# Kernel tuning notes

Measured on AMD Instinct MI355X. Metric: run time of the kernel, lower is better.

The kernel has to match this reference:

```python
import jax, jax.numpy as jnp
import numpy as np
from jax import lax

DIM = 96
B, S = 2, 48
EPS_LN = 1e-6
EPS_GRN = 1e-6


def setup_inputs() -> dict:
    key = jax.random.key(0)
    ks = jax.random.split(key, 11)
    d, h = DIM, 4 * DIM
    return {
        "x": jax.random.normal(ks[0], (B, d, S, S, S), jnp.float32),
        "dw_w": jax.random.normal(ks[1], (d, 1, 7, 7, 7), jnp.float32) * 0.05,  # (O, I/groups, kD,kH,kW)
        "dw_b": jax.random.normal(ks[2], (d,), jnp.float32) * 0.02,
        "ln_w": jnp.ones((d,), jnp.float32),
        "ln_b": jnp.zeros((d,), jnp.float32),
        "w1": jax.random.normal(ks[3], (d, h), jnp.float32) * 0.02,
        "b1": jax.random.normal(ks[4], (h,), jnp.float32) * 0.02,
        "grn_w": jax.random.normal(ks[5], (h,), jnp.float32) * 0.02,
        "grn_b": jax.random.normal(ks[6], (h,), jnp.float32) * 0.02,
        "w2": jax.random.normal(ks[7], (h, d), jnp.float32) * 0.02,
        "b2": jax.random.normal(ks[8], (d,), jnp.float32) * 0.02,
    }


def reference(x, dw_w, dw_b, ln_w, ln_b, w1, b1, grn_w, grn_b, w2, b2):
    # depthwise 7x7x7 conv, padding 3, groups = channels; x: (B, C, D, H, W)
    y = lax.conv_general_dilated(
        x, dw_w, window_strides=(1, 1, 1), padding=[(3, 3)] * 3,
        dimension_numbers=("NCDHW", "OIDHW", "NCDHW"), feature_group_count=DIM,
    ) + dw_b[None, :, None, None, None]
    # channels_last: (B, D, H, W, C)
    h = jnp.transpose(y, (0, 2, 3, 4, 1))
    # LayerNorm over channel dim
    mu = jnp.mean(h, axis=-1, keepdims=True)
    var = jnp.mean((h - mu) ** 2, axis=-1, keepdims=True)
    h = (h - mu) * lax.rsqrt(var + EPS_LN) * ln_w + ln_b
    # pointwise MLP expand + GELU (exact, erf-based, like torch)
    h = jnp.einsum("bdhwc,ce->bdhwe", h, w1) + b1
    h = jax.nn.gelu(h, approximate=False)
    # GRN: global L2 norm over spatial dims (1,2,3), per channel
    g = jnp.sqrt(jnp.sum(h * h, axis=(1, 2, 3), keepdims=True))  # (B,1,1,1,4C)
    n = g / (jnp.mean(g, axis=-1, keepdims=True) + EPS_GRN)
    h = grn_w * (h * n) + grn_b + h
    # pointwise MLP contract
    h = jnp.einsum("bdhwe,ec->bdhwc", h, w2) + b2
    # back to channels_first + residual
    return x + jnp.transpose(h, (0, 4, 1, 2, 3))
```

## Files before the change

kernel.cpp:

```cpp
#include <hip/hip_runtime.h>
#include <hip/hip_bf16.h>
#include <string.h>

#define S3 110592
#define CDIM 96
#define EDIM 384
#define ZIN 14
#define YIN 22

typedef __attribute__((ext_vector_type(8))) short bf16x8;
typedef __attribute__((ext_vector_type(4))) float f32x4;
typedef unsigned short ushort_t;

__device__ __forceinline__ ushort_t f2bf(float f) {
  __hip_bfloat16 h = __float2bfloat16(f);
  union { __hip_bfloat16 h; ushort_t u; } cv; cv.h = h; return cv.u;
}
__device__ __forceinline__ float bf2f(ushort_t u) {
  union { __hip_bfloat16 h; ushort_t u; } cv; cv.u = u; return __bfloat162float(cv.h);
}

__global__ void kprep(const float* __restrict__ ln_w, const float* __restrict__ ln_b,
                      const float* __restrict__ w1, const float* __restrict__ b1,
                      const float* __restrict__ grn_b, const float* __restrict__ w2,
                      const float* __restrict__ b2,
                      ushort_t* __restrict__ w1p, float* __restrict__ b1f, float* __restrict__ bias2) {
  int idx = blockIdx.x * 256 + threadIdx.x;
  if (idx < 24 * 3 * 64 * 8) {
    int j = idx & 7, lane = (idx >> 3) & 63, ks = (idx >> 9) % 3, nt = idx / 1536;
    int c = ks * 32 + (lane >> 4) * 8 + j;
    int e = nt * 16 + (lane & 15);
    w1p[idx] = f2bf(ln_w[c] * w1[c * EDIM + e]);
  }
  if (idx < EDIM) {
    float s = b1[idx];
    for (int c = 0; c < CDIM; ++c) s += ln_b[c] * w1[c * EDIM + idx];
    b1f[idx] = s;
  }
  if (idx < CDIM) {
    float s = b2[idx];
    for (int e = 0; e < EDIM; ++e) s += grn_b[e] * w2[e * CDIM + idx];
    bias2[idx] = s;
  }
}

__global__ void kpackB(const float* __restrict__ dw_w, ushort_t* __restrict__ Btab) {
  int idx = blockIdx.x * 256 + threadIdx.x;
  if (idx >= 96 * 49 * 512) return;
  int pos = idx & 511; int t = (idx >> 9) % 49; int c = idx / (49 * 512);
  int lane = pos >> 3, j = pos & 7;
  int k = (lane >> 4) * 8 + j, n = lane & 15;
  int tx = k - n - 1;
  int tz = t / 7, ty = t % 7;
  float v = (tx >= 0 && tx < 7) ? dw_w[c * 343 + tz * 49 + ty * 7 + tx] : 0.f;
  Btab[idx] = f2bf(v);
}

template<int HALF>
__device__ __forceinline__ void conv_ty_loop(const unsigned* tile, const ushort_t* Bt,
                                             int lane, int am, int xg, f32x4* acc) {
#pragma unroll 1
  for (int ty = 0; ty < 7; ++ty) {
    bf16x8 bfr[7];
#pragma unroll
    for (int tz = 0; tz < 7; ++tz)
      bfr[tz] = *(const bf16x8*)&Bt[(tz * 7 + ty) * 512 + lane * 8];
    int rowbase = am + ty;
#pragma unroll
    for (int zl = 0; zl < 7; ++zl) {
      int row = (HALF * 7 + zl) * YIN + rowbase;
      int byteoff = (row << 7) + (xg ^ ((row & 7) << 4));
      bf16x8 af = *(const bf16x8*)((const char*)tile + byteoff);
#pragma unroll
      for (int tz = 0; tz < 7; ++tz) {
        int l = (HALF == 0) ? (zl - tz) : (zl + 6 - tz);
        if (l >= 0 && l < 7)
          acc[l] = __builtin_amdgcn_mfma_f32_16x16x32_bf16(af, bfr[tz], acc[l], 0, 0, 0);
      }
    }
  }
}

__global__ __launch_bounds__(384, 6) void kconv(const float* __restrict__ x,
                                                const ushort_t* __restrict__ Btab,
                                                const float* __restrict__ dw_b,
                                                ushort_t* __restrict__ y) {
  __shared__ unsigned tile[ZIN * YIN * 32];
  int bid = blockIdx.x;
  int xcd = bid & 7, wi = bid >> 3;
  int c = xcd * 12 + wi / 36;
  int rr_ = wi % 36;
  int b = rr_ / 18;
  int t_ = rr_ % 18;
  int zt = t_ / 3, yt = t_ % 3;
  int z0 = zt * 8, y0 = yt * 16;
  size_t base = (size_t)(b * 96 + c) * S3;
  int tid = threadIdx.x;

  for (int i = tid; i < 308 * 8; i += 384) {
    int row = i >> 3; int pe = i & 7;
    int pc = (pe < 2) ? pe : pe + 24;
    tile[(row << 5) + (pc ^ ((row & 7) << 2))] = 0u;
  }
#pragma unroll 4
  for (int i = tid; i < 308 * 24; i += 384) {
    int row = i / 24; int pc = 2 + (i - row * 24);
    int dz = row / YIN, dy = row - dz * YIN;
    int gz = z0 - 3 + dz, gy = y0 - 3 + dy;
    float2 v = make_float2(0.f, 0.f);
    if ((unsigned)gz < 48u && (unsigned)gy < 48u)
      v = *(const float2*)&x[base + (size_t)gz * 2304 + gy * 48 + 2 * pc - 4];
    tile[(row << 5) + (pc ^ ((row & 7) << 2))] = (unsigned)f2bf(v.x) | ((unsigned)f2bf(v.y) << 16);
  }
  __syncthreads();

  int w = tid >> 6;
  int X = w % 3, half = w / 3;
  int lane = tid & 63;
  int am = lane & 15, g = lane >> 4;
  int xg = X * 32 + g * 16;

  f32x4 acc[7];
#pragma unroll
  for (int p = 0; p < 7; ++p) acc[p] = (f32x4){0.f, 0.f, 0.f, 0.f};

  const ushort_t* __restrict__ Bt = Btab + (size_t)c * 49 * 512;
  if (half == 0) conv_ty_loop<0>(tile, Bt, lane, am, xg, acc);
  else           conv_ty_loop<1>(tile, Bt, lane, am, xg, acc);

  float bv = dw_b[c];
  float* red = (float*)tile;
  int rcol = X * 16 + am;
  __syncthreads();
  if (half == 0) {
#pragma unroll
    for (int l = 1; l < 7; ++l)
#pragma unroll
      for (int r = 0; r < 4; ++r)
        red[(l - 1) * 800 + (g * 4 + r) * 50 + rcol] = acc[l][r];
  }
  __syncthreads();
  if (half == 0) {
    size_t zb = base + (size_t)z0 * 2304;
#pragma unroll
    for (int r = 0; r < 4; ++r)
      y[zb + (size_t)(y0 + g * 4 + r) * 48 + rcol] = f2bf(acc[0][r] + bv);
  } else {
#pragma unroll
    for (int l = 0; l < 7; ++l) {
      size_t zb = base + (size_t)(z0 + l + 1) * 2304;
#pragma unroll
      for (int r = 0; r < 4; ++r) {
        float v = acc[l][r] + bv;
        if (l < 6) v += red[l * 800 + (g * 4 + r) * 50 + rcol];
        y[zb + (size_t)(y0 + g * 4 + r) * 48 + rcol] = f2bf(v);
      }
    }
  }
}

__global__ __launch_bounds__(512, 4) void kmlp1(const ushort_t* __restrict__ y,
                                                const ushort_t* __restrict__ w1p,
                                                const float* __restrict__ b1f,
                                                ushort_t* __restrict__ h,
                                                float* __restrict__ sumsq) {
  __shared__ ushort_t Al[64 * 104];
  __shared__ float red_s[8][64], red_q[8][64];
  __shared__ float stat_mu[64], stat_rv[64];
  __shared__ float ssq_s[EDIM];
  int tid = threadIdx.x;
  int q = tid >> 6, lane = tid & 63;
  size_t pos0 = (size_t)blockIdx.x * 64;
  int b = (int)(pos0 / S3);
  int sp0 = (int)(pos0 % S3);

  bf16x8 bfg[3][3];
#pragma unroll
  for (int ntl = 0; ntl < 3; ++ntl)
#pragma unroll
    for (int ks = 0; ks < 3; ++ks)
      bfg[ntl][ks] = *(const bf16x8*)&w1p[(size_t)(((q * 3 + ntl) * 3 + ks) * 64 + lane) * 8];

  float v[12];
  float s = 0.f, ss = 0.f;
  const ushort_t* yb = y + (size_t)b * 96 * S3 + sp0 + lane;
#pragma unroll
  for (int i = 0; i < 12; ++i) {
    float f = bf2f(yb[(size_t)(q * 12 + i) * S3]);
    v[i] = f; s += f; ss += f * f;
  }
  red_s[q][lane] = s; red_q[q][lane] = ss;
  __syncthreads();
  if (tid < 64) {
    float su = 0.f, sq = 0.f;
#pragma unroll
    for (int k = 0; k < 8; ++k) { su += red_s[k][tid]; sq += red_q[k][tid]; }
    float mu = su * (1.f / 96.f);
    float var = sq * (1.f / 96.f) - mu * mu;
    stat_mu[tid] = mu;
    stat_rv[tid] = rsqrtf(var + 1e-6f);
  }
  __syncthreads();
  {
    float mu = stat_mu[lane], rv = stat_rv[lane];
#pragma unroll
    for (int i4 = 0; i4 < 3; ++i4) {
      ushort_t u0 = f2bf((v[i4 * 4 + 0] - mu) * rv);
      ushort_t u1 = f2bf((v[i4 * 4 + 1] - mu) * rv);
      ushort_t u2 = f2bf((v[i4 * 4 + 2] - mu) * rv);
      ushort_t u3 = f2bf((v[i4 * 4 + 3] - mu) * rv);
      uint2 t; t.x = (unsigned)u0 | ((unsigned)u1 << 16); t.y = (unsigned)u2 | ((unsigned)u3 << 16);
      *(uint2*)&Al[lane * 104 + q * 12 + i4 * 4] = t;
    }
  }
  __syncthreads();

  f32x4 acc[4][3];
#pragma unroll
  for (int mt = 0; mt < 4; ++mt)
#pragma unroll
    for (int ntl = 0; ntl < 3; ++ntl) acc[mt][ntl] = (f32x4){0.f, 0.f, 0.f, 0.f};

  int row = lane & 15, g = lane >> 4;
#pragma unroll
  for (int ks = 0; ks < 3; ++ks) {
    bf16x8 af[4];
    int colb = ks * 32 + g * 8;
#pragma unroll
    for (int mt = 0; mt < 4; ++mt)
      af[mt] = *(const bf16x8*)&Al[(mt * 16 + row) * 104 + colb];
#pragma unroll
    for (int ntl = 0; ntl < 3; ++ntl) {
#pragma unroll
      for (int mt = 0; mt < 4; ++mt)
        acc[mt][ntl] = __builtin_amdgcn_mfma_f32_16x16x32_bf16(af[mt], bfg[ntl][ks], acc[mt][ntl], 0, 0, 0);
    }
  }

#pragma unroll
  for (int ntl = 0; ntl < 3; ++ntl) {
    int e = q * 48 + ntl * 16 + row;
    float bb = b1f[e];
    float ssq = 0.f;
#pragma unroll
    for (int mt = 0; mt < 4; ++mt) {
#pragma unroll
      for (int r = 0; r < 4; ++r) {
        float val = acc[mt][ntl][r] + bb;
        float gel = 0.5f * val * (1.f + erff(val * 0.70710678118f));
        size_t p = pos0 + mt * 16 + g * 4 + r;
        h[p * EDIM + e] = f2bf(gel);
        ssq += gel * gel;
      }
    }
    ssq += __shfl_xor(ssq, 16, 64);
    ssq += __shfl_xor(ssq, 32, 64);
    if (g == 0) ssq_s[e] = ssq;
  }
  __syncthreads();
  if (tid < EDIM) atomicAdd(&sumsq[b * EDIM + tid], ssq_s[tid]);
}

__global__ void kscale(const float* __restrict__ sumsq, const float* __restrict__ grn_w,
                       float* __restrict__ scale) {
  __shared__ float wsum[6];
  __shared__ float mean_s;
  int b = blockIdx.x, e = threadIdx.x;
  float gv = sqrtf(sumsq[b * EDIM + e]);
  float t = gv;
#pragma unroll
  for (int off = 1; off <= 32; off <<= 1) t += __shfl_xor(t, off, 64);
  if ((e & 63) == 0) wsum[e >> 6] = t;
  __syncthreads();
  if (e == 0) {
    float m = 0.f;
    for (int i = 0; i < 6; ++i) m += wsum[i];
    mean_s = m * (1.f / EDIM);
  }
  __syncthreads();
  scale[b * EDIM + e] = grn_w[e] * (gv / (mean_s + 1e-6f)) + 1.f;
}

__global__ void kpackw2(const float* __restrict__ scale, const float* __restrict__ w2,
                        ushort_t* __restrict__ w2s) {
  int idx = blockIdx.x * 256 + threadIdx.x;
  int b = idx / 36864; int r = idx % 36864;
  int j = r & 7, lane = (r >> 3) & 63, ks = (r >> 9) % 12, nt = r / 6144;
  int e = ks * 32 + (lane >> 4) * 8 + j, cc = nt * 16 + (lane & 15);
  w2s[idx] = f2bf(scale[b * EDIM + e] * w2[e * CDIM + cc]);
}

__global__ __launch_bounds__(256, 4) void kmlp2(const ushort_t* __restrict__ h,
                                                const ushort_t* __restrict__ w2s,
                                                const float* __restrict__ bias2,
                                                const float* __restrict__ x,
                                                float* __restrict__ out) {
  __shared__ float tile[96 * 65];
  int tid = threadIdx.x;
  int w = tid >> 6, lane = tid & 63;
  size_t pos0 = (size_t)blockIdx.x * 128;
  int b = (int)(pos0 / S3);
  int sp0 = (int)(pos0 % S3);
  int row = lane & 15, g = lane >> 4;

  f32x4 acc[2][6];
#pragma unroll
  for (int hf = 0; hf < 2; ++hf)
#pragma unroll
    for (int nt = 0; nt < 6; ++nt) acc[hf][nt] = (f32x4){0.f, 0.f, 0.f, 0.f};

  const ushort_t* w2b = w2s + (size_t)b * 36864;
  size_t abase0 = (pos0 + w * 16 + row) * (size_t)EDIM + g * 8;
  size_t abase1 = abase0 + (size_t)64 * EDIM;
#pragma unroll
  for (int ks = 0; ks < 12; ++ks) {
    bf16x8 af0 = *(const bf16x8*)&h[abase0 + ks * 32];
    bf16x8 af1 = *(const bf16x8*)&h[abase1 + ks * 32];
#pragma unroll
    for (int nt = 0; nt < 6; ++nt) {
      bf16x8 bfg = *(const bf16x8*)&w2b[(size_t)((nt * 12 + ks) * 64 + lane) * 8];
      acc[0][nt] = __builtin_amdgcn_mfma_f32_16x16x32_bf16(af0, bfg, acc[0][nt], 0, 0, 0);
      acc[1][nt] = __builtin_amdgcn_mfma_f32_16x16x32_bf16(af1, bfg, acc[1][nt], 0, 0, 0);
    }
  }

#pragma unroll
  for (int hf = 0; hf < 2; ++hf) {
    __syncthreads();
#pragma unroll
    for (int nt = 0; nt < 6; ++nt) {
      int cc = nt * 16 + row;
#pragma unroll
      for (int r = 0; r < 4; ++r)
        tile[cc * 65 + w * 16 + g * 4 + r] = acc[hf][nt][r];
    }
    __syncthreads();
#pragma unroll
    for (int k = 0; k < 12; ++k) {
      int idx = tid + k * 256;
      int cc = idx >> 5, pp = (idx & 31) * 2;
      size_t o = (size_t)(b * 96 + cc) * S3 + sp0 + hf * 64 + pp;
      float2 xv = *(const float2*)&x[o];
      float bb = bias2[cc];
      float2 ov;
      ov.x = xv.x + tile[cc * 65 + pp] + bb;
      ov.y = xv.y + tile[cc * 65 + pp + 1] + bb;
      *(float2*)&out[o] = ov;
    }
  }
}

extern "C" void kernel_launch(void* const* d_in, const int* in_sizes, int n_in,
                              void* d_out, int out_size, void* d_ws, size_t ws_size,
                              hipStream_t stream) {
  const float* x     = (const float*)d_in[0];
  const float* dw_w  = (const float*)d_in[1];
  const float* dw_b  = (const float*)d_in[2];
  const float* ln_w  = (const float*)d_in[3];
  const float* ln_b  = (const float*)d_in[4];
  const float* w1    = (const float*)d_in[5];
  const float* b1    = (const float*)d_in[6];
  const float* grn_w = (const float*)d_in[7];
  const float* grn_b = (const float*)d_in[8];
  const float* w2    = (const float*)d_in[9];
  const float* b2    = (const float*)d_in[10];
  float* out = (float*)d_out;

  char* ws = (char*)d_ws;
  size_t off = 0;
  auto alloc = [&](size_t bytes) -> void* {
    void* p = ws + off;
    off = (off + bytes + 511) & ~(size_t)511;
    return p;
  };
  ushort_t* y    = (ushort_t*)alloc((size_t)2 * 96 * S3 * 2);
  ushort_t* h    = (ushort_t*)alloc((size_t)221184 * EDIM * 2);
  ushort_t* w1p  = (ushort_t*)alloc(36864 * 2);
  ushort_t* w2s  = (ushort_t*)alloc((size_t)2 * 36864 * 2);
  ushort_t* Btab = (ushort_t*)alloc((size_t)96 * 49 * 512 * 2);
  float* b1f     = (float*)alloc(EDIM * 4);
  float* bias2   = (float*)alloc(CDIM * 4);
  float* sumsq   = (float*)alloc(2 * EDIM * 4);
  float* scale   = (float*)alloc(2 * EDIM * 4);

  hipMemsetAsync(sumsq, 0, 2 * EDIM * 4, stream);
  kprep<<<145, 256, 0, stream>>>(ln_w, ln_b, w1, b1, grn_b, w2, b2, w1p, b1f, bias2);
  kpackB<<<9408, 256, 0, stream>>>(dw_w, Btab);
  kconv<<<3456, 384, 0, stream>>>(x, Btab, dw_b, y);
  kmlp1<<<3456, 512, 0, stream>>>(y, w1p, b1f, h, sumsq);
  kscale<<<2, 384, 0, stream>>>(sumsq, grn_w, scale);
  kpackw2<<<288, 256, 0, stream>>>(scale, w2, w2s);
  kmlp2<<<1728, 256, 0, stream>>>(h, w2s, bias2, x, out);
}
```

Baseline: 337.7 us.

## Recompute MLP expand in fused kernel instead of storing hidden activations

After: 307.2 us. 1.1x faster.

```diff
diff --git a/kernel.cpp b/kernel.cpp
--- a/kernel.cpp
+++ b/kernel.cpp
@@ -18,6 +18,11 @@
 }
 __device__ __forceinline__ float bf2f(ushort_t u) {
   union { __hip_bfloat16 h; ushort_t u; } cv; cv.u = u; return __bfloat162float(cv.h);
+}
+__device__ __forceinline__ float gelu_fast(float v) {
+  float u = v * (-1.59576912f - 0.07135481f * v * v);
+  float s = __expf(u);
+  return __fdividef(v, 1.f + s);
 }
 
 __global__ void kprep(const float* __restrict__ ln_w, const float* __restrict__ ln_b,
@@ -159,11 +164,10 @@
   }
 }
 
-__global__ __launch_bounds__(512, 4) void kmlp1(const ushort_t* __restrict__ y,
-                                                const ushort_t* __restrict__ w1p,
-                                                const float* __restrict__ b1f,
-                                                ushort_t* __restrict__ h,
-                                                float* __restrict__ sumsq) {
+__global__ __launch_bounds__(512, 4) void ksum(const ushort_t* __restrict__ y,
+                                               const ushort_t* __restrict__ w1p,
+                                               const float* __restrict__ b1f,
+                                               float* __restrict__ sumsq) {
   __shared__ ushort_t Al[64 * 104];
   __shared__ float red_s[8][64], red_q[8][64];
   __shared__ float stat_mu[64], stat_rv[64];
@@ -246,10 +250,7 @@
     for (int mt = 0; mt < 4; ++mt) {
 #pragma unroll
       for (int r = 0; r < 4; ++r) {
-        float val = acc[mt][ntl][r] + bb;
-        float gel = 0.5f * val * (1.f + erff(val * 0.70710678118f));
-        size_t p = pos0 + mt * 16 + g * 4 + r;
-        h[p * EDIM + e] = f2bf(gel);
+        float gel = gelu_fast(acc[mt][ntl][r] + bb);
         ssq += gel * gel;
       }
     }
@@ -290,63 +291,138 @@
   w2s[idx] = f2bf(scale[b * EDIM + e] * w2[e * CDIM + cc]);
 }
 
-__global__ __launch_bounds__(256, 4) void kmlp2(const ushort_t* __restrict__ h,
-                                                const ushort_t* __restrict__ w2s,
-                                                const float* __restrict__ bias2,
-                                                const float* __restrict__ x,
-                                                float* __restrict__ out) {
-  __shared__ float tile[96 * 65];
+__global__ __launch_bounds__(512, 4) void kfused(const ushort_t* __restrict__ y,
+                                                 const ushort_t* __restrict__ w1p,
+                                                 const float* __restrict__ b1f,
+                                                 const ushort_t* __restrict__ w2s,
+                                                 const float* __restrict__ bias2,
+                                                 const float* __restrict__ x,
+                                                 float* __restrict__ out) {
+  __shared__ __align__(16) char smem[68096];
+  ushort_t* Al   = (ushort_t*)smem;
+  float* red_s   = (float*)(smem + 13312);
+  float* red_q   = (float*)(smem + 15360);
+  float* stat_mu = (float*)(smem + 17408);
+  float* stat_rv = (float*)(smem + 17664);
+  ushort_t* htile= (ushort_t*)(smem + 17920);
+  float* otile   = (float*)(smem + 17920);
+
   int tid = threadIdx.x;
-  int w = tid >> 6, lane = tid & 63;
-  size_t pos0 = (size_t)blockIdx.x * 128;
+  int q = tid >> 6, lane = tid & 63;
+  size_t pos0 = (size_t)blockIdx.x * 64;
   int b = (int)(pos0 / S3);
   int sp0 = (int)(pos0 % S3);
   int row = lane & 15, g = lane >> 4;
 
-  f32x4 acc[2][6];
-#pragma unroll
-  for (int hf = 0; hf < 2; ++hf)
-#pragma unroll
-    for (int nt = 0; nt < 6; ++nt) acc[hf][nt] = (f32x4){0.f, 0.f, 0.f, 0.f};
-
+  float v[12];
+  float s = 0.f, ss = 0.f;
+  const ushort_t* yb = y + (size_t)b * 96 * S3 + sp0 + lane;
+#pragma unroll
+  for (int i = 0; i < 12; ++i) {
+    float f = bf2f(yb[(size_t)(q * 12 + i) * S3]);
+    v[i] = f; s += f; ss += f * f;
+  }
+  red_s[q * 64 + lane] = s; red_q[q * 64 + lane] = ss;
+  __syncthreads();
+  if (tid < 64) {
+    float su = 0.f, sq = 0.f;
+#pragma unroll
+    for (int k = 0; k < 8; ++k) { su += red_s[k * 64 + tid]; sq += red_q[k * 64 + tid]; }
+    float mu = su * (1.f / 96.f);
+    float var = sq * (1.f / 96.f) - mu * mu;
+    stat_mu[tid] = mu;
+    stat_rv[tid] = rsqrtf(var + 1e-6f);
+  }
+  __syncthreads();
+  {
+    float mu = stat_mu[lane], rv = stat_rv[lane];
+#pragma unroll
+    for (int i4 = 0; i4 < 3; ++i4) {
+      ushort_t u0 = f2bf((v[i4 * 4 + 0] - mu) * rv);
+      ushort_t u1 = f2bf((v[i4 * 4 + 1] - mu) * rv);
+      ushort_t u2 = f2bf((v[i4 * 4 + 2] - mu) * rv);
+      ushort_t u3 = f2bf((v[i4 * 4 + 3] - mu) * rv);
+      uint2 t; t.x = (unsigned)u0 | ((unsigned)u1 << 16); t.y = (unsigned)u2 | ((unsigned)u3 << 16);
+      *(uint2*)&Al[lane * 104 + q * 12 + i4 * 4] = t;
+    }
+  }
+  __syncthreads();
+
+  f32x4 acc[4][3];
+#pragma unroll
+  for (int mt = 0; mt < 4; ++mt)
+#pragma unroll
+    for (int ntl = 0; ntl < 3; ++ntl) acc[mt][ntl] = (f32x4){0.f, 0.f, 0.f, 0.f};
+
+#pragma unroll
+  for (int ks = 0; ks < 3; ++ks) {
+    bf16x8 af[4];
+    int colb = ks * 32 + g * 8;
+#pragma unroll
+    for (int mt = 0; mt < 4; ++mt)
+      af[mt] = *(const bf16x8*)&Al[(mt * 16 + row) * 104 + colb];
+#pragma unroll
+    for (int ntl = 0; ntl < 3; ++ntl) {
+      bf16x8 bfg = *(const bf16x8*)&w1p[(size_t)(((q * 3 + ntl) * 3 + ks) * 64 + lane) * 8];
+#pragma unroll
+      for (int mt = 0; mt < 4; ++mt)
+        acc[mt][ntl] = __builtin_amdgcn_mfma_f32_16x16x32_bf16(af[mt], bfg, acc[mt][ntl], 0, 0, 0);
+    }
+  }
+
+#pragma unroll
+  for (int ntl = 0; ntl < 3; ++ntl) {
+    int e = q * 48 + ntl * 16 + row;
+    float bb = b1f[e];
+#pragma unroll
+    for (int mt = 0; mt < 4; ++mt) {
+#pragma unroll
+      for (int r = 0; r < 4; ++r) {
+        float gel = gelu_fast(acc[mt][ntl][r] + bb);
+        htile[(mt * 16 + g * 4 + r) * 392 + e] = f2bf(gel);
+      }
+    }
+  }
+  __syncthreads();
+
+  int mt2 = q & 3, nh = q >> 2;
+  f32x4 acc2[3];
+#pragma unroll
+  for (int ntl = 0; ntl < 3; ++ntl) acc2[ntl] = (f32x4){0.f, 0.f, 0.f, 0.f};
   const ushort_t* w2b = w2s + (size_t)b * 36864;
-  size_t abase0 = (pos0 + w * 16 + row) * (size_t)EDIM + g * 8;
-  size_t abase1 = abase0 + (size_t)64 * EDIM;
+  const ushort_t* arow = &htile[(mt2 * 16 + row) * 392];
 #pragma unroll
   for (int ks = 0; ks < 12; ++ks) {
-    bf16x8 af0 = *(const bf16x8*)&h[abase0 + ks * 32];
-    bf16x8 af1 = *(const bf16x8*)&h[abase1 + ks * 32];
-#pragma unroll
-    for (int nt = 0; nt < 6; ++nt) {
-      bf16x8 bfg = *(const bf16x8*)&w2b[(size_t)((nt * 12 + ks) * 64 + lane) * 8];
-      acc[0][nt] = __builtin_amdgcn_mfma_f32_16x16x32_bf16(af0, bfg, acc[0][nt], 0, 0, 0);
-      acc[1][nt] = __builtin_amdgcn_mfma_f32_16x16x32_bf16(af1, bfg, acc[1][nt], 0, 0, 0);
-    }
-  }
-
-#pragma unroll
-  for (int hf = 0; hf < 2; ++hf) {
-    __syncthreads();
-#pragma unroll
-    for (int nt = 0; nt < 6; ++nt) {
-      int cc = nt * 16 + row;
-#pragma unroll
-      for (int r = 0; r < 4; ++r)
-        tile[cc * 65 + w * 16 + g * 4 + r] = acc[hf][nt][r];
-    }
-    __syncthreads();
-#pragma unroll
-    for (int k = 0; k < 12; ++k) {
-      int idx = tid + k * 256;
-      int cc = idx >> 5, pp = (idx & 31) * 2;
-      size_t o = (size_t)(b * 96 + cc) * S3 + sp0 + hf * 64 + pp;
-      float2 xv = *(const float2*)&x[o];
-      float bb = bias2[cc];
-      float2 ov;
-      ov.x = xv.x + tile[cc * 65 + pp] + bb;
-      ov.y = xv.y + tile[cc * 65 + pp + 1] + bb;
-      *(float2*)&out[o] = ov;
-    }
+    bf16x8 af2 = *(const bf16x8*)&arow[g * 8 + ks * 32];
+#pragma unroll
+    for (int ntl = 0; ntl < 3; ++ntl) {
+      int nt = nh * 3 + ntl;
+      bf16x8 bfg2 = *(const bf16x8*)&w2b[(size_t)((nt * 12 + ks) * 64 + lane) * 8];
+      acc2[ntl] = __builtin_amdgcn_mfma_f32_16x16x32_bf16(af2, bfg2, acc2[ntl], 0, 0, 0);
+    }
+  }
+  __syncthreads();
+
+#pragma unroll
+  for (int ntl = 0; ntl < 3; ++ntl) {
+    int cc = (nh * 3 + ntl) * 16 + row;
+#pragma unroll
+    for (int r = 0; r < 4; ++r)
+      otile[cc * 65 + mt2 * 16 + g * 4 + r] = acc2[ntl][r];
+  }
+  __syncthreads();
+
+#pragma unroll
+  for (int k = 0; k < 6; ++k) {
+    int idx = tid + k * 512;
+    int cc = idx >> 5, pp = (idx & 31) * 2;
+    size_t o = (size_t)(b * 96 + cc) * S3 + sp0 + pp;
+    float2 xv = *(const float2*)&x[o];
+    float bb = bias2[cc];
+    float2 ov;
+    ov.x = xv.x + otile[cc * 65 + pp] + bb;
+    ov.y = xv.y + otile[cc * 65 + pp + 1] + bb;
+    *(float2*)&out[o] = ov;
   }
 }
 
@@ -374,7 +450,6 @@
     return p;
   };
   ushort_t* y    = (ushort_t*)alloc((size_t)2 * 96 * S3 * 2);
-  ushort_t* h    = (ushort_t*)alloc((size_t)221184 * EDIM * 2);
   ushort_t* w1p  = (ushort_t*)alloc(36864 * 2);
   ushort_t* w2s  = (ushort_t*)alloc((size_t)2 * 36864 * 2);
   ushort_t* Btab = (ushort_t*)alloc((size_t)96 * 49 * 512 * 2);
@@ -387,8 +462,8 @@
   kprep<<<145, 256, 0, stream>>>(ln_w, ln_b, w1, b1, grn_b, w2, b2, w1p, b1f, bias2);
   kpackB<<<9408, 256, 0, stream>>>(dw_w, Btab);
   kconv<<<3456, 384, 0, stream>>>(x, Btab, dw_b, y);
-  kmlp1<<<3456, 512, 0, stream>>>(y, w1p, b1f, h, sumsq);
+  ksum<<<3456, 512, 0, stream>>>(y, w1p, b1f, sumsq);
   kscale<<<2, 384, 0, stream>>>(sumsq, grn_w, scale);
   kpackw2<<<288, 256, 0, stream>>>(scale, w2, w2s);
-  kmlp2<<<1728, 256, 0, stream>>>(h, w2s, bias2, x, out);
-}
+  kfused<<<3456, 512, 0, stream>>>(y, w1p, b1f, w2s, bias2, x, out);
+}
```
